# Kernel tuning notes

Hardware: AMD Instinct MI355X
Metric: run time of the kernel (lower is better)

The kernel has to match this reference:

```python
import jax, jax.numpy as jnp
import numpy as np

D_MODEL = 1024
D_FF = 4096
N_EXP = 8
TOP_K = 2


def _gelu(x):
    # torch F.gelu default is exact (erf) gelu
    return jax.nn.gelu(x, approximate=False)


def setup_inputs() -> dict:
    key = jax.random.key(0)
    ks = jax.random.split(key, 12)
    s = 0.02
    return {
        "x": jax.random.normal(ks[0], (4, 2048, D_MODEL), dtype=jnp.float32),
        "shared_w1": jax.random.normal(ks[1], (D_MODEL, D_FF), dtype=jnp.float32) * s,
        "shared_b1": jnp.zeros((D_FF,), jnp.float32),
        "shared_w2": jax.random.normal(ks[2], (D_FF, D_MODEL), dtype=jnp.float32) * s,
        "shared_b2": jnp.zeros((D_MODEL,), jnp.float32),
        "router_w": jax.random.normal(ks[3], (D_MODEL, N_EXP), dtype=jnp.float32) * s,
        "router_b": jnp.zeros((N_EXP,), jnp.float32),
        "exp_w1": jax.random.normal(ks[4], (N_EXP, D_MODEL, D_FF), dtype=jnp.float32) * s,
        "exp_b1": jnp.zeros((N_EXP, D_FF), jnp.float32),
        "exp_w2": jax.random.normal(ks[5], (N_EXP, D_FF, D_MODEL), dtype=jnp.float32) * s,
        "exp_b2": jnp.zeros((N_EXP, D_MODEL), jnp.float32),
    }


def reference(x, shared_w1, shared_b1, shared_w2, shared_b2,
              router_w, router_b, exp_w1, exp_b1, exp_w2, exp_b2):
    leading = x.shape[:-1]
    d = x.shape[-1]
    xf = x.reshape(-1, d)                                   # [T, d]
    T = xf.shape[0]

    # always-on shared FFN
    h_shared = _gelu(xf @ shared_w1 + shared_b1) @ shared_w2 + shared_b2  # [T, d]

    # router: softmax -> top-k -> renormalize
    logits = xf @ router_w + router_b                       # [T, E]
    routing = jax.nn.softmax(logits, axis=-1)
    sel_w, sel_idx = jax.lax.top_k(routing, TOP_K)          # [T, K]
    sel_w = sel_w / (jnp.sum(sel_w, axis=-1, keepdims=True) + 1e-9)

    # dense combine weights: w[t,e] = sum_k sel_w[t,k] * [sel_idx[t,k]==e]
    combine = jnp.zeros((T, N_EXP), routing.dtype)
    combine = combine.at[jnp.arange(T)[:, None], sel_idx].add(sel_w)

    # specialist residual: sum_e combine[:,e] * FFN_e(x)
    residual = jnp.zeros_like(xf)
    for e in range(N_EXP):                                  # fixed small expert loop
        h = _gelu(xf @ exp_w1[e] + exp_b1[e])               # [T, d_ff]
        y = h @ exp_w2[e] + exp_b2[e]                       # [T, d]
        residual = residual + combine[:, e:e + 1] * y

    out = h_shared + residual
    return out.reshape(*leading, d)
```

## Files before the change

### kernel.cpp

```cpp
#include <hip/hip_runtime.h>
#include <hip/hip_bf16.h>


#define D_MODEL 1024
#define D_FF    4096
#define N_EXP   8
#define T_TOK   8192
#define BK      64

typedef _Float16 half8  __attribute__((ext_vector_type(8)));
typedef _Float16 half4v __attribute__((ext_vector_type(4)));
typedef float    floatx4 __attribute__((ext_vector_type(4)));

__device__ __forceinline__ float gelu_exact(float x) {
  return 0.5f * x * (1.0f + erff(x * 0.70710678118654752f));
}

__device__ __forceinline__ void gld_lds16(const _Float16* g, _Float16* l) {
  __builtin_amdgcn_global_load_lds(
      (const __attribute__((address_space(1))) void*)g,
      (__attribute__((address_space(3))) void*)l, 16, 0, 0);
}

__global__ void convert_f32_f16(const float* __restrict__ src,
                                _Float16* __restrict__ dst, int n4) {
  int i = blockIdx.x * blockDim.x + threadIdx.x;
  if (i >= n4) return;
  float4 v = ((const float4*)src)[i];
  half4v h;
  h[0] = (_Float16)v.x; h[1] = (_Float16)v.y;
  h[2] = (_Float16)v.z; h[3] = (_Float16)v.w;
  ((half4v*)dst)[i] = h;
}

__global__ void transpose_convert9(const float* __restrict__ srcSh,
                                   const float* __restrict__ srcEx,
                                   _Float16* __restrict__ dst, int R, int C) {
  const size_t msz = (size_t)R * C;
  const float* src = (blockIdx.z == 0) ? srcSh : srcEx + msz * (blockIdx.z - 1);
  _Float16* d = dst + msz * blockIdx.z;
  __shared__ float tile[32][33];
  int c0 = blockIdx.x * 32, r0 = blockIdx.y * 32;
  int tx = threadIdx.x, ty = threadIdx.y;
#pragma unroll
  for (int i = 0; i < 4; ++i)
    tile[ty + i * 8][tx] = src[(size_t)(r0 + ty + i * 8) * C + c0 + tx];
  __syncthreads();
#pragma unroll
  for (int i = 0; i < 4; ++i)
    d[(size_t)(c0 + ty + i * 8) * R + r0 + tx] = (_Float16)tile[tx][ty + i * 8];
}

__global__ void router_kernel(const float* __restrict__ x,
                              const float* __restrict__ rw,
                              const float* __restrict__ rb,
                              int* __restrict__ sel_idx,
                              float* __restrict__ sel_w,
                              int* __restrict__ counts) {
  int lane = threadIdx.x & 63;
  int t = blockIdx.x * 4 + (threadIdx.x >> 6);
  const float* xr = x + (size_t)t * D_MODEL;
  float acc[N_EXP];
#pragma unroll
  for (int e = 0; e < N_EXP; ++e) acc[e] = 0.f;
  for (int k = lane; k < D_MODEL; k += 64) {
    float xv = xr[k];
    const float* w = rw + (size_t)k * N_EXP;
#pragma unroll
    for (int e = 0; e < N_EXP; ++e) acc[e] += xv * w[e];
  }
#pragma unroll
  for (int off = 32; off > 0; off >>= 1) {
#pragma unroll
    for (int e = 0; e < N_EXP; ++e)
      acc[e] += __shfl_down(acc[e], off, 64);
  }
  if (lane == 0) {
    float mx = -1e30f;
#pragma unroll
    for (int e = 0; e < N_EXP; ++e) { acc[e] += rb[e]; mx = fmaxf(mx, acc[e]); }
    float p[N_EXP], s = 0.f;
#pragma unroll
    for (int e = 0; e < N_EXP; ++e) { p[e] = expf(acc[e] - mx); s += p[e]; }
    float inv = 1.f / s;
#pragma unroll
    for (int e = 0; e < N_EXP; ++e) p[e] *= inv;
    int i0 = 0; float p0 = p[0];
#pragma unroll
    for (int e = 1; e < N_EXP; ++e) if (p[e] > p0) { p0 = p[e]; i0 = e; }
    int i1 = -1; float p1 = -1.f;
#pragma unroll
    for (int e = 0; e < N_EXP; ++e)
      if (e != i0 && p[e] > p1) { p1 = p[e]; i1 = e; }
    float s2 = p0 + p1 + 1e-9f;
    sel_idx[2 * t] = i0; sel_idx[2 * t + 1] = i1;
    sel_w[2 * t] = p0 / s2; sel_w[2 * t + 1] = p1 / s2;
    atomicAdd(&counts[i0 * 32], 1);
    atomicAdd(&counts[i1 * 32], 1);
  }
}

__global__ void scan_kernel(const int* __restrict__ counts,
                            int* __restrict__ offsets,
                            int* __restrict__ cursor) {
  if (threadIdx.x == 0) {
    int s = 0;
    for (int e = 0; e < N_EXP; ++e) {
      offsets[e] = s; cursor[e * 32] = s; s += counts[e * 32];
    }
    offsets[N_EXP] = s;
  }
}

__global__ void assign_kernel(const int* __restrict__ sel_idx,
                              int* __restrict__ cursor,
                              int* __restrict__ rows,
                              int* __restrict__ inv) {
  int t = blockIdx.x * blockDim.x + threadIdx.x;
  if (t >= T_TOK) return;
#pragma unroll
  for (int k = 0; k < 2; ++k) {
    int e = sel_idx[2 * t + k];
    int pos = atomicAdd(&cursor[e * 32], 1);
    rows[pos] = t;
    inv[2 * t + k] = pos;
  }
}

template <int PHASE>
__global__ __launch_bounds__(256, 3) void gemm_kernel(
    const _Float16* __restrict__ A, const _Float16* __restrict__ Wt,
    const float* __restrict__ biasSh, const float* __restrict__ biasEx,
    _Float16* __restrict__ Hout, float* __restrict__ out,
    float* __restrict__ Yexp, const int* __restrict__ rows,
    const int* __restrict__ counts, const int* __restrict__ offsets) {
  constexpr int K = (PHASE == 1) ? D_MODEL : D_FF;
  constexpr int N = (PHASE == 1) ? D_FF : D_MODEL;
  const int z = blockIdx.z;
  int M = T_TOK, offs = 0;
  if (z > 0) {
    M = counts[(z - 1) * 32];
    offs = offsets[z - 1];
    if ((int)blockIdx.y * 128 >= M) return;
  }
  const int tid = threadIdx.x, lane = tid & 63, wid = tid >> 6;
  const int m0 = blockIdx.y * 128, n0 = blockIdx.x * 128;
  const _Float16* Wz = Wt + (size_t)z * N * K;

  __shared__ __align__(16) _Float16 As[128 * BK];
  __shared__ __align__(16) _Float16 Bs[128 * BK];

  const int sub = lane >> 3, pp = lane & 7, g = pp ^ sub;

  int r0i = m0 + (wid * 4 + 0) * 8 + sub;
  int r1i = m0 + (wid * 4 + 1) * 8 + sub;
  int r2i = m0 + (wid * 4 + 2) * 8 + sub;
  int r3i = m0 + (wid * 4 + 3) * 8 + sub;
  size_t gr0, gr1, gr2, gr3;
  if (z == 0) {
    gr0 = (size_t)r0i; gr1 = (size_t)r1i; gr2 = (size_t)r2i; gr3 = (size_t)r3i;
  } else if constexpr (PHASE == 1) {
    gr0 = (size_t)rows[offs + (r0i < M ? r0i : M - 1)];
    gr1 = (size_t)rows[offs + (r1i < M ? r1i : M - 1)];
    gr2 = (size_t)rows[offs + (r2i < M ? r2i : M - 1)];
    gr3 = (size_t)rows[offs + (r3i < M ? r3i : M - 1)];
  } else {
    gr0 = (size_t)(T_TOK + offs + (r0i < M ? r0i : M - 1));
    gr1 = (size_t)(T_TOK + offs + (r1i < M ? r1i : M - 1));
    gr2 = (size_t)(T_TOK + offs + (r2i < M ? r2i : M - 1));
    gr3 = (size_t)(T_TOK + offs + (r3i < M ? r3i : M - 1));
  }
  const _Float16* aS0 = A + gr0 * K + g * 8;
  const _Float16* aS1 = A + gr1 * K + g * 8;
  const _Float16* aS2 = A + gr2 * K + g * 8;
  const _Float16* aS3 = A + gr3 * K + g * 8;
  const _Float16* bS0 = Wz + (size_t)(n0 + (wid * 4 + 0) * 8 + sub) * K + g * 8;
  const _Float16* bS1 = Wz + (size_t)(n0 + (wid * 4 + 1) * 8 + sub) * K + g * 8;
  const _Float16* bS2 = Wz + (size_t)(n0 + (wid * 4 + 2) * 8 + sub) * K + g * 8;
  const _Float16* bS3 = Wz + (size_t)(n0 + (wid * 4 + 3) * 8 + sub) * K + g * 8;

  floatx4 acc[4][4] = {};
  const int wm = wid >> 1, wn = wid & 1;
  const int lr = lane & 15, qd = lane >> 4;

  for (int kt = 0; kt < K; kt += BK) {
    __syncthreads();
    gld_lds16(aS0, As + (wid * 4 + 0) * 512);
    gld_lds16(aS1, As + (wid * 4 + 1) * 512);
    gld_lds16(aS2, As + (wid * 4 + 2) * 512);
    gld_lds16(aS3, As + (wid * 4 + 3) * 512);
    gld_lds16(bS0, Bs + (wid * 4 + 0) * 512);
    gld_lds16(bS1, Bs + (wid * 4 + 1) * 512);
    gld_lds16(bS2, Bs + (wid * 4 + 2) * 512);
    gld_lds16(bS3, Bs + (wid * 4 + 3) * 512);
    aS0 += BK; aS1 += BK; aS2 += BK; aS3 += BK;
    bS0 += BK; bS1 += BK; bS2 += BK; bS3 += BK;
    asm volatile("s_waitcnt vmcnt(0)" ::: "memory");
    __syncthreads();
#pragma unroll
    for (int h = 0; h < 2; ++h) {
      half8 af[4], bf[4];
#pragma unroll
      for (int mi = 0; mi < 4; ++mi) {
        const int r = wm * 64 + mi * 16 + lr;
        const int slot = (h * 4 + qd) ^ (r & 7);
        af[mi] = *(const half8*)(As + r * BK + slot * 8);
      }
#pragma unroll
      for (int ni = 0; ni < 4; ++ni) {
        const int r = wn * 64 + ni * 16 + lr;
        const int slot = (h * 4 + qd) ^ (r & 7);
        bf[ni] = *(const half8*)(Bs + r * BK + slot * 8);
      }
#pragma unroll
      for (int mi = 0; mi < 4; ++mi)
#pragma unroll
        for (int ni = 0; ni < 4; ++ni)
          acc[mi][ni] = __builtin_amdgcn_mfma_f32_16x16x32_f16(
              af[mi], bf[ni], acc[mi][ni], 0, 0, 0);
    }
  }

  const float* be = (z == 0) ? biasSh : biasEx + (size_t)(z - 1) * N;
#pragma unroll
  for (int mi = 0; mi < 4; ++mi) {
#pragma unroll
    for (int ni = 0; ni < 4; ++ni) {
      floatx4 v = acc[mi][ni];
#pragma unroll
      for (int r4 = 0; r4 < 4; ++r4) {
        const int lrow = m0 + wm * 64 + mi * 16 + qd * 4 + r4;
        const int col = n0 + wn * 64 + ni * 16 + lr;
        const float val = v[r4] + be[col];
        if constexpr (PHASE == 1) {
          if (z == 0) {
            Hout[(size_t)lrow * N + col] = (_Float16)gelu_exact(val);
          } else if (lrow < M) {
            Hout[(size_t)(T_TOK + offs + lrow) * N + col] =
                (_Float16)gelu_exact(val);
          }
        } else {
          if (z == 0) {
            out[(size_t)lrow * N + col] = val;
          } else if (lrow < M) {
            Yexp[(size_t)(offs + lrow) * N + col] = val;
          }
        }
      }
    }
  }
}

__global__ void combine_kernel(float* __restrict__ out,
                               const float* __restrict__ Yexp,
                               const int* __restrict__ inv,
                               const float* __restrict__ selw) {
  const int t = blockIdx.x;
  const int c = threadIdx.x * 4;
  const int p0 = inv[2 * t], p1 = inv[2 * t + 1];
  const float w0 = selw[2 * t], w1 = selw[2 * t + 1];
  float4 o = *(float4*)(out + (size_t)t * D_MODEL + c);
  const float4 a = *(const float4*)(Yexp + (size_t)p0 * D_MODEL + c);
  const float4 b = *(const float4*)(Yexp + (size_t)p1 * D_MODEL + c);
  o.x += w0 * a.x + w1 * b.x;
  o.y += w0 * a.y + w1 * b.y;
  o.z += w0 * a.z + w1 * b.z;
  o.w += w0 * a.w + w1 * b.w;
  *(float4*)(out + (size_t)t * D_MODEL + c) = o;
}

extern "C" void kernel_launch(void* const* d_in, const int* in_sizes, int n_in,
                              void* d_out, int out_size, void* d_ws,
                              size_t ws_size, hipStream_t stream) {
  const float* x   = (const float*)d_in[0];
  const float* sw1 = (const float*)d_in[1];
  const float* sb1 = (const float*)d_in[2];
  const float* sw2 = (const float*)d_in[3];
  const float* sb2 = (const float*)d_in[4];
  const float* rw  = (const float*)d_in[5];
  const float* rb  = (const float*)d_in[6];
  const float* ew1 = (const float*)d_in[7];
  const float* eb1 = (const float*)d_in[8];
  const float* ew2 = (const float*)d_in[9];
  const float* eb2 = (const float*)d_in[10];
  float* out = (float*)d_out;

  char* ws = (char*)d_ws;
  size_t off = 0;
  auto alloc = [&](size_t bytes) {
    void* p = ws + off;
    off += (bytes + 255) & ~(size_t)255;
    return p;
  };
  _Float16* xb  = (_Float16*)alloc((size_t)T_TOK * D_MODEL * 2);
  _Float16* w2t = (_Float16*)alloc((size_t)9 * D_MODEL * D_FF * 2);
  _Float16* H   = (_Float16*)alloc((size_t)3 * T_TOK * D_FF * 2);
  _Float16* w1t = (_Float16*)alloc((size_t)9 * D_FF * D_MODEL * 2);
  float* Yexp   = (float*)w1t;
  int*   sel_idx = (int*)alloc((size_t)T_TOK * 2 * 4);
  float* sel_w   = (float*)alloc((size_t)T_TOK * 2 * 4);
  int*   rows    = (int*)alloc((size_t)2 * T_TOK * 4);
  int*   inv     = (int*)alloc((size_t)2 * T_TOK * 4);
  int*   counts  = (int*)alloc(N_EXP * 32 * 4);
  int*   offsets = (int*)alloc(16 * 4);
  int*   cursor  = (int*)alloc(N_EXP * 32 * 4);
  (void)ws_size; (void)in_sizes; (void)n_in; (void)out_size;

  hipMemsetAsync(counts, 0, N_EXP * 32 * 4, stream);

  convert_f32_f16<<<(T_TOK * D_MODEL / 4 + 255) / 256, 256, 0, stream>>>(
      x, xb, T_TOK * D_MODEL / 4);
  dim3 tb(32, 8);
  transpose_convert9<<<dim3(D_FF / 32, D_MODEL / 32, 9), tb, 0, stream>>>(
      sw1, ew1, w1t, D_MODEL, D_FF);
  transpose_convert9<<<dim3(D_MODEL / 32, D_FF / 32, 9), tb, 0, stream>>>(
      sw2, ew2, w2t, D_FF, D_MODEL);

  router_kernel<<<T_TOK / 4, 256, 0, stream>>>(x, rw, rb, sel_idx, sel_w, counts);
  scan_kernel<<<1, 64, 0, stream>>>(counts, offsets, cursor);
  assign_kernel<<<T_TOK / 256, 256, 0, stream>>>(sel_idx, cursor, rows, inv);

  gemm_kernel<1><<<dim3(D_FF / 128, T_TOK / 128, 9), 256, 0, stream>>>(
      xb, w1t, sb1, eb1, H, nullptr, nullptr, rows, counts, offsets);
  gemm_kernel<2><<<dim3(D_MODEL / 128, T_TOK / 128, 9), 256, 0, stream>>>(
      H, w2t, sb2, eb2, nullptr, out, Yexp, rows, counts, offsets);

  combine_kernel<<<T_TOK, 256, 0, stream>>>(out, Yexp, inv, sel_w);
}
```

Baseline: 1.073 ms.

## Use 256x256 tiles with 8 waves and double-buffered LDS prefetch in GEMMs

```diff
diff --git a/kernel.cpp b/kernel.cpp
--- a/kernel.cpp
+++ b/kernel.cpp
@@ -128,7 +128,7 @@
 }
 
 template <int PHASE>
-__global__ __launch_bounds__(256, 3) void gemm_kernel(
+__global__ __launch_bounds__(512, 2) void gemm_kernel(
     const _Float16* __restrict__ A, const _Float16* __restrict__ Wt,
     const float* __restrict__ biasSh, const float* __restrict__ biasEx,
     _Float16* __restrict__ Hout, float* __restrict__ out,
@@ -136,100 +136,111 @@
     const int* __restrict__ counts, const int* __restrict__ offsets) {
   constexpr int K = (PHASE == 1) ? D_MODEL : D_FF;
   constexpr int N = (PHASE == 1) ? D_FF : D_MODEL;
+  constexpr int NT = K / BK;
   const int z = blockIdx.z;
   int M = T_TOK, offs = 0;
   if (z > 0) {
     M = counts[(z - 1) * 32];
     offs = offsets[z - 1];
-    if ((int)blockIdx.y * 128 >= M) return;
+    if ((int)blockIdx.y * 256 >= M) return;
   }
   const int tid = threadIdx.x, lane = tid & 63, wid = tid >> 6;
-  const int m0 = blockIdx.y * 128, n0 = blockIdx.x * 128;
+  const int m0 = blockIdx.y * 256, n0 = blockIdx.x * 256;
   const _Float16* Wz = Wt + (size_t)z * N * K;
 
-  __shared__ __align__(16) _Float16 As[128 * BK];
-  __shared__ __align__(16) _Float16 Bs[128 * BK];
+  __shared__ __align__(16) _Float16 As[2 * 256 * BK];
+  __shared__ __align__(16) _Float16 Bs[2 * 256 * BK];
 
   const int sub = lane >> 3, pp = lane & 7, g = pp ^ sub;
 
-  int r0i = m0 + (wid * 4 + 0) * 8 + sub;
-  int r1i = m0 + (wid * 4 + 1) * 8 + sub;
-  int r2i = m0 + (wid * 4 + 2) * 8 + sub;
-  int r3i = m0 + (wid * 4 + 3) * 8 + sub;
-  size_t gr0, gr1, gr2, gr3;
-  if (z == 0) {
-    gr0 = (size_t)r0i; gr1 = (size_t)r1i; gr2 = (size_t)r2i; gr3 = (size_t)r3i;
-  } else if constexpr (PHASE == 1) {
-    gr0 = (size_t)rows[offs + (r0i < M ? r0i : M - 1)];
-    gr1 = (size_t)rows[offs + (r1i < M ? r1i : M - 1)];
-    gr2 = (size_t)rows[offs + (r2i < M ? r2i : M - 1)];
-    gr3 = (size_t)rows[offs + (r3i < M ? r3i : M - 1)];
-  } else {
-    gr0 = (size_t)(T_TOK + offs + (r0i < M ? r0i : M - 1));
-    gr1 = (size_t)(T_TOK + offs + (r1i < M ? r1i : M - 1));
-    gr2 = (size_t)(T_TOK + offs + (r2i < M ? r2i : M - 1));
-    gr3 = (size_t)(T_TOK + offs + (r3i < M ? r3i : M - 1));
-  }
-  const _Float16* aS0 = A + gr0 * K + g * 8;
-  const _Float16* aS1 = A + gr1 * K + g * 8;
-  const _Float16* aS2 = A + gr2 * K + g * 8;
-  const _Float16* aS3 = A + gr3 * K + g * 8;
-  const _Float16* bS0 = Wz + (size_t)(n0 + (wid * 4 + 0) * 8 + sub) * K + g * 8;
-  const _Float16* bS1 = Wz + (size_t)(n0 + (wid * 4 + 1) * 8 + sub) * K + g * 8;
-  const _Float16* bS2 = Wz + (size_t)(n0 + (wid * 4 + 2) * 8 + sub) * K + g * 8;
-  const _Float16* bS3 = Wz + (size_t)(n0 + (wid * 4 + 3) * 8 + sub) * K + g * 8;
-
-  floatx4 acc[4][4] = {};
-  const int wm = wid >> 1, wn = wid & 1;
+  const _Float16* aS[4];
+  const _Float16* bS[4];
+#pragma unroll
+  for (int j = 0; j < 4; ++j) {
+    int r = m0 + wid * 32 + j * 8 + sub;
+    size_t gr;
+    if (z == 0) {
+      gr = (size_t)r;
+    } else {
+      int rc = r < M ? r : M - 1;
+      if constexpr (PHASE == 1) gr = (size_t)rows[offs + rc];
+      else                      gr = (size_t)(T_TOK + offs + rc);
+    }
+    aS[j] = A + gr * K + g * 8;
+    bS[j] = Wz + (size_t)(n0 + wid * 32 + j * 8 + sub) * K + g * 8;
+  }
+
+#pragma unroll
+  for (int j = 0; j < 4; ++j) {
+    gld_lds16(aS[j], As + (wid * 4 + j) * 512); aS[j] += BK;
+  }
+#pragma unroll
+  for (int j = 0; j < 4; ++j) {
+    gld_lds16(bS[j], Bs + (wid * 4 + j) * 512); bS[j] += BK;
+  }
+
+  floatx4 acc[8][4] = {};
+  const int wm = wid >> 2, wn = wid & 3;
   const int lr = lane & 15, qd = lane >> 4;
-
-  for (int kt = 0; kt < K; kt += BK) {
-    __syncthreads();
-    gld_lds16(aS0, As + (wid * 4 + 0) * 512);
-    gld_lds16(aS1, As + (wid * 4 + 1) * 512);
-    gld_lds16(aS2, As + (wid * 4 + 2) * 512);
-    gld_lds16(aS3, As + (wid * 4 + 3) * 512);
-    gld_lds16(bS0, Bs + (wid * 4 + 0) * 512);
-    gld_lds16(bS1, Bs + (wid * 4 + 1) * 512);
-    gld_lds16(bS2, Bs + (wid * 4 + 2) * 512);
-    gld_lds16(bS3, Bs + (wid * 4 + 3) * 512);
-    aS0 += BK; aS1 += BK; aS2 += BK; aS3 += BK;
-    bS0 += BK; bS1 += BK; bS2 += BK; bS3 += BK;
-    asm volatile("s_waitcnt vmcnt(0)" ::: "memory");
-    __syncthreads();
-#pragma unroll
-    for (int h = 0; h < 2; ++h) {
-      half8 af[4], bf[4];
-#pragma unroll
-      for (int mi = 0; mi < 4; ++mi) {
-        const int r = wm * 64 + mi * 16 + lr;
-        const int slot = (h * 4 + qd) ^ (r & 7);
-        af[mi] = *(const half8*)(As + r * BK + slot * 8);
+  const int xm = lr & 7;
+
+#pragma unroll 2
+  for (int t = 0; t < NT; ++t) {
+    _Float16* Ac = As + (t & 1) * (256 * BK);
+    _Float16* Bc = Bs + (t & 1) * (256 * BK);
+    _Float16* An = As + ((t & 1) ^ 1) * (256 * BK);
+    _Float16* Bn = Bs + ((t & 1) ^ 1) * (256 * BK);
+    if (t + 1 < NT) {
+#pragma unroll
+      for (int j = 0; j < 4; ++j) {
+        gld_lds16(aS[j], An + (wid * 4 + j) * 512); aS[j] += BK;
       }
-#pragma unroll
-      for (int ni = 0; ni < 4; ++ni) {
-        const int r = wn * 64 + ni * 16 + lr;
-        const int slot = (h * 4 + qd) ^ (r & 7);
-        bf[ni] = *(const half8*)(Bs + r * BK + slot * 8);
-      }
-#pragma unroll
-      for (int mi = 0; mi < 4; ++mi)
+      asm volatile("s_waitcnt vmcnt(4)" ::: "memory");
+    } else {
+      asm volatile("s_waitcnt vmcnt(0)" ::: "memory");
+    }
+    __builtin_amdgcn_s_barrier();
+    asm volatile("" ::: "memory");
+    __builtin_amdgcn_sched_barrier(0);
+#pragma unroll
+    for (int ks = 0; ks < 2; ++ks) {
+      half8 af[8], bf[4];
+      const int slot = (ks * 4 + qd) ^ xm;
+#pragma unroll
+      for (int mi = 0; mi < 8; ++mi)
+        af[mi] = *(const half8*)(Ac + (wm * 128 + mi * 16 + lr) * BK + slot * 8);
+#pragma unroll
+      for (int ni = 0; ni < 4; ++ni)
+        bf[ni] = *(const half8*)(Bc + (wn * 64 + ni * 16 + lr) * BK + slot * 8);
+      __builtin_amdgcn_s_setprio(1);
+#pragma unroll
+      for (int mi = 0; mi < 8; ++mi)
 #pragma unroll
         for (int ni = 0; ni < 4; ++ni)
           acc[mi][ni] = __builtin_amdgcn_mfma_f32_16x16x32_f16(
               af[mi], bf[ni], acc[mi][ni], 0, 0, 0);
-    }
+      __builtin_amdgcn_s_setprio(0);
+      if (ks == 0 && t + 1 < NT) {
+#pragma unroll
+        for (int j = 0; j < 4; ++j) {
+          gld_lds16(bS[j], Bn + (wid * 4 + j) * 512); bS[j] += BK;
+        }
+      }
+    }
+    asm volatile("s_waitcnt lgkmcnt(0)" ::: "memory");
+    __builtin_amdgcn_sched_barrier(0);
+    __builtin_amdgcn_s_barrier();
   }
 
   const float* be = (z == 0) ? biasSh : biasEx + (size_t)(z - 1) * N;
 #pragma unroll
-  for (int mi = 0; mi < 4; ++mi) {
+  for (int mi = 0; mi < 8; ++mi) {
 #pragma unroll
     for (int ni = 0; ni < 4; ++ni) {
       floatx4 v = acc[mi][ni];
 #pragma unroll
       for (int r4 = 0; r4 < 4; ++r4) {
-        const int lrow = m0 + wm * 64 + mi * 16 + qd * 4 + r4;
+        const int lrow = m0 + wm * 128 + mi * 16 + qd * 4 + r4;
         const int col = n0 + wn * 64 + ni * 16 + lr;
         const float val = v[r4] + be[col];
         if constexpr (PHASE == 1) {
@@ -320,9 +331,9 @@
   scan_kernel<<<1, 64, 0, stream>>>(counts, offsets, cursor);
   assign_kernel<<<T_TOK / 256, 256, 0, stream>>>(sel_idx, cursor, rows, inv);
 
-  gemm_kernel<1><<<dim3(D_FF / 128, T_TOK / 128, 9), 256, 0, stream>>>(
+  gemm_kernel<1><<<dim3(D_FF / 256, T_TOK / 256, 9), 512, 0, stream>>>(
       xb, w1t, sb1, eb1, H, nullptr, nullptr, rows, counts, offsets);
-  gemm_kernel<2><<<dim3(D_MODEL / 128, T_TOK / 128, 9), 256, 0, stream>>>(
+  gemm_kernel<2><<<dim3(D_MODEL / 256, T_TOK / 256, 9), 512, 0, stream>>>(
       H, w2t, sb2, eb2, nullptr, out, Yexp, rows, counts, offsets);
 
   combine_kernel<<<T_TOK, 256, 0, stream>>>(out, Yexp, inv, sel_w);
```

New measurement: 1.214 ms. +13.1%, slower.

## Switch GEMM to 32x32x16 MFMA and remap block indices for L2 locality

Applied to the files above, without the earlier changes.

```diff
diff --git a/kernel.cpp b/kernel.cpp
--- a/kernel.cpp
+++ b/kernel.cpp
@@ -10,7 +10,7 @@
 
 typedef _Float16 half8  __attribute__((ext_vector_type(8)));
 typedef _Float16 half4v __attribute__((ext_vector_type(4)));
-typedef float    floatx4 __attribute__((ext_vector_type(4)));
+typedef float    floatx16 __attribute__((ext_vector_type(16)));
 
 __device__ __forceinline__ float gelu_exact(float x) {
   return 0.5f * x * (1.0f + erff(x * 0.70710678118654752f));
@@ -136,15 +136,21 @@
     const int* __restrict__ counts, const int* __restrict__ offsets) {
   constexpr int K = (PHASE == 1) ? D_MODEL : D_FF;
   constexpr int N = (PHASE == 1) ? D_FF : D_MODEL;
+  constexpr int GX = N / 128;
+  constexpr int CPX = GX / 8;
+  const int L = (int)blockIdx.y * GX + (int)blockIdx.x;
+  const int bx = (L & 7) * CPX + ((L >> 3) % CPX);
+  const int by = (L >> 3) / CPX;
+
   const int z = blockIdx.z;
   int M = T_TOK, offs = 0;
   if (z > 0) {
     M = counts[(z - 1) * 32];
     offs = offsets[z - 1];
-    if ((int)blockIdx.y * 128 >= M) return;
+    if (by * 128 >= M) return;
   }
   const int tid = threadIdx.x, lane = tid & 63, wid = tid >> 6;
-  const int m0 = blockIdx.y * 128, n0 = blockIdx.x * 128;
+  const int m0 = by * 128, n0 = bx * 128;
   const _Float16* Wz = Wt + (size_t)z * N * K;
 
   __shared__ __align__(16) _Float16 As[128 * BK];
@@ -179,9 +185,10 @@
   const _Float16* bS2 = Wz + (size_t)(n0 + (wid * 4 + 2) * 8 + sub) * K + g * 8;
   const _Float16* bS3 = Wz + (size_t)(n0 + (wid * 4 + 3) * 8 + sub) * K + g * 8;
 
-  floatx4 acc[4][4] = {};
+  floatx16 acc[2][2] = {};
   const int wm = wid >> 1, wn = wid & 1;
-  const int lr = lane & 15, qd = lane >> 4;
+  const int l31 = lane & 31, lh = lane >> 5;
+  const int x7 = l31 & 7;
 
   for (int kt = 0; kt < K; kt += BK) {
     __syncthreads();
@@ -198,52 +205,51 @@
     asm volatile("s_waitcnt vmcnt(0)" ::: "memory");
     __syncthreads();
 #pragma unroll
-    for (int h = 0; h < 2; ++h) {
-      half8 af[4], bf[4];
-#pragma unroll
-      for (int mi = 0; mi < 4; ++mi) {
-        const int r = wm * 64 + mi * 16 + lr;
-        const int slot = (h * 4 + qd) ^ (r & 7);
-        af[mi] = *(const half8*)(As + r * BK + slot * 8);
-      }
-#pragma unroll
-      for (int ni = 0; ni < 4; ++ni) {
-        const int r = wn * 64 + ni * 16 + lr;
-        const int slot = (h * 4 + qd) ^ (r & 7);
-        bf[ni] = *(const half8*)(Bs + r * BK + slot * 8);
-      }
-#pragma unroll
-      for (int mi = 0; mi < 4; ++mi)
-#pragma unroll
-        for (int ni = 0; ni < 4; ++ni)
-          acc[mi][ni] = __builtin_amdgcn_mfma_f32_16x16x32_f16(
+    for (int ks = 0; ks < 4; ++ks) {
+      const int slot = ((ks * 2 + lh) ^ x7) * 8;
+      half8 af[2], bf[2];
+#pragma unroll
+      for (int mi = 0; mi < 2; ++mi)
+        af[mi] = *(const half8*)(As + (wm * 64 + mi * 32 + l31) * BK + slot);
+#pragma unroll
+      for (int ni = 0; ni < 2; ++ni)
+        bf[ni] = *(const half8*)(Bs + (wn * 64 + ni * 32 + l31) * BK + slot);
+#pragma unroll
+      for (int mi = 0; mi < 2; ++mi)
+#pragma unroll
+        for (int ni = 0; ni < 2; ++ni)
+          acc[mi][ni] = __builtin_amdgcn_mfma_f32_32x32x16_f16(
               af[mi], bf[ni], acc[mi][ni], 0, 0, 0);
     }
   }
 
   const float* be = (z == 0) ? biasSh : biasEx + (size_t)(z - 1) * N;
 #pragma unroll
-  for (int mi = 0; mi < 4; ++mi) {
-#pragma unroll
-    for (int ni = 0; ni < 4; ++ni) {
-      floatx4 v = acc[mi][ni];
+  for (int mi = 0; mi < 2; ++mi) {
+#pragma unroll
+    for (int ni = 0; ni < 2; ++ni) {
+      floatx16 v = acc[mi][ni];
+      const int col = n0 + wn * 64 + ni * 32 + l31;
+      const float bias = be[col];
 #pragma unroll
       for (int r4 = 0; r4 < 4; ++r4) {
-        const int lrow = m0 + wm * 64 + mi * 16 + qd * 4 + r4;
-        const int col = n0 + wn * 64 + ni * 16 + lr;
-        const float val = v[r4] + be[col];
-        if constexpr (PHASE == 1) {
-          if (z == 0) {
-            Hout[(size_t)lrow * N + col] = (_Float16)gelu_exact(val);
-          } else if (lrow < M) {
-            Hout[(size_t)(T_TOK + offs + lrow) * N + col] =
-                (_Float16)gelu_exact(val);
-          }
-        } else {
-          if (z == 0) {
-            out[(size_t)lrow * N + col] = val;
-          } else if (lrow < M) {
-            Yexp[(size_t)(offs + lrow) * N + col] = val;
+#pragma unroll
+        for (int j = 0; j < 4; ++j) {
+          const int lrow = m0 + wm * 64 + mi * 32 + 4 * lh + 8 * r4 + j;
+          const float val = v[r4 * 4 + j] + bias;
+          if constexpr (PHASE == 1) {
+            if (z == 0) {
+              Hout[(size_t)lrow * N + col] = (_Float16)gelu_exact(val);
+            } else if (lrow < M) {
+              Hout[(size_t)(T_TOK + offs + lrow) * N + col] =
+                  (_Float16)gelu_exact(val);
+            }
+          } else {
+            if (z == 0) {
+              out[(size_t)lrow * N + col] = val;
+            } else if (lrow < M) {
+              Yexp[(size_t)(offs + lrow) * N + col] = val;
+            }
           }
         }
       }
```

Result: slower. 1.108 ms (+3.2%).
